# Kernel tuning notes

Measured on AMD Instinct MI355X. Metric: run time of the kernel, lower is better.

Reference implementation:

```python
import jax, jax.numpy as jnp
import numpy as np

K = 3
STRIDE = 2
SQRT_D = 4  # in_d_capsules = 16 -> 4x4 matrix pose
LN_EPS = 1e-5


def _unfold(x, k, s):
    # x: [B, N, H, W, A] -> [B, N, k, k, Hout, Wout, A] (matches torch unfold+permute)
    B, N, H, W, A = x.shape
    Hout = (H - k) // s + 1
    Wout = (W - k) // s + 1
    hi = jnp.arange(Hout) * s
    wi = jnp.arange(Wout) * s
    x1 = x[:, :, hi[:, None] + jnp.arange(k)[None, :]]            # [B,N,Hout,k,W,A]
    x2 = x1[:, :, :, :, wi[:, None] + jnp.arange(k)[None, :]]     # [B,N,Hout,k,Wout,k,A]
    return jnp.transpose(x2, (0, 1, 3, 5, 2, 4, 6))               # [B,N,k,k,Hout,Wout,A]


def setup_inputs() -> dict:
    key = jax.random.key(0)
    k1, k2, k3 = jax.random.split(key, 3)
    B, N_in, H, W, D_in = 32, 32, 32, 32, 16
    N_out, D_out = 32, 16
    Hout = (H - K) // STRIDE + 1
    Wout = (W - K) // STRIDE + 1
    w_const = np.sqrt(N_out / (SQRT_D * N_in * K * K)).astype(np.float32)
    return {
        "input": jax.random.normal(k1, (B, N_in, H, W, D_in), dtype=jnp.float32),
        "next_capsule_value": jax.random.normal(k2, (B, N_out, Hout, Wout, D_out), dtype=jnp.float32),
        "w": w_const * jax.random.normal(k3, (K, K, N_in, SQRT_D, SQRT_D, N_out), dtype=jnp.float32),
        "gamma": jnp.ones((D_out,), dtype=jnp.float32),
        "beta": jnp.zeros((D_out,), dtype=jnp.float32),
        "num_iter": 1,
    }


def reference(input, next_capsule_value, w, gamma, beta, num_iter):
    out_d = SQRT_D * SQRT_D
    scale = 1.0 / np.sqrt(out_d).astype(np.float32)
    inp = _unfold(input, K, STRIDE)                                # [B,N,k,k,h,w,A]
    B, N, _, _, h, wd, A = inp.shape
    _inp = inp.reshape(B, N, K, K, h, wd, SQRT_D, SQRT_D)          # bnklhwax
    M = next_capsule_value.shape[1]
    ncv = next_capsule_value.reshape(B, M, h, wd, SQRT_D, SQRT_D)  # bmhwad
    # query-key routing logits
    qk = jnp.einsum('bnklhwax,klnxdm,bmhwad->bnklmhw', _inp, w, ncv) * scale
    qk = jax.nn.softmax(qk, axis=4)
    qk = qk / (jnp.sum(qk, axis=4, keepdims=True) + 1e-10)
    # value aggregation
    out = jnp.einsum('bnklmhw,bnklhwax,klnxdm->bmhwad', qk, _inp, w)
    out = out.reshape(B, M, h, wd, out_d)
    # dropout p=0 -> identity; LayerNorm over capsule dim
    mu = jnp.mean(out, axis=-1, keepdims=True)
    var = jnp.var(out, axis=-1, keepdims=True)
    out = (out - mu) / jnp.sqrt(var + LN_EPS) * gamma + beta
    return out
```

## Files before the change

### kernel.cpp

```cpp
#include <hip/hip_runtime.h>

#define HOUT 15
#define WOUT 15

typedef float v2 __attribute__((ext_vector_type(2)));

#define DPP_ADDF(x, ctrl) \
    ((x) + __builtin_bit_cast(float, __builtin_amdgcn_update_dpp( \
        0, __builtin_bit_cast(int, (x)), (ctrl), 0xF, 0xF, true)))

__global__ __launch_bounds__(256) void prep_w(const float* __restrict__ wt,
                                              float* __restrict__ w2)
{
    const int t  = blockIdx.x * 256 + threadIdx.x;
    const int d  = t & 3;
    const int m  = (t >> 2) & 31;
    const int x  = (t >> 7) & 3;
    const int r  = t >> 9;
    const int kl = r % 9;
    const int n  = r / 9;
    w2[t] = wt[((((kl * 32 + n) * 4 + x) * 4 + d) * 32) + m];
}

__global__ __launch_bounds__(128, 4) void caps_fused(
    const float* __restrict__ input,
    const float* __restrict__ ncv,
    const float* __restrict__ w2,
    const float* __restrict__ gamma,
    const float* __restrict__ beta,
    float* __restrict__ out)
{
    const int tid  = threadIdx.x;
    const int grp  = tid >> 5;
    const int lane = tid & 31;

    const int pos = blockIdx.x * 4 + grp;
    const int b   = pos / (HOUT * WOUT);
    const int hw  = pos % (HOUT * WOUT);
    const int h   = hw / WOUT;
    const int wo  = hw % WOUT;
    const int h0  = h * 2, w0 = wo * 2;

    const float* ncv_p = ncv + ((((size_t)b * 32 + lane) * HOUT + h) * WOUT + wo) * 16;
    v2 cv2[8];
#pragma unroll
    for (int j = 0; j < 8; ++j) cv2[j] = *(const v2*)(ncv_p + j * 2);

    v2 acc2[8];
#pragma unroll
    for (int j = 0; j < 8; ++j) acc2[j] = (v2){0.0f, 0.0f};

    const float* ip0 = input + ((((size_t)b * 32) * 32 + h0) * 32 + w0) * 16;
    const float* wp0 = w2 + lane * 4;

    for (int n = 0; n < 32; ++n) {
        const float* ipn = ip0 + (size_t)n * 16384;
        const float* wpn = wp0 + (size_t)n * 4608;

#pragma unroll
        for (int kl = 0; kl < 9; ++kl) {
            const int k = kl / 3, l = kl % 3;
            const float* ip = ipn + (k * 32 + l) * 16;

            float av[16];
#pragma unroll
            for (int j = 0; j < 16; j += 4) {
                float4 t4 = *(const float4*)(ip + j);
                av[j] = t4.x; av[j + 1] = t4.y; av[j + 2] = t4.z; av[j + 3] = t4.w;
            }

            const float* wp = wpn + kl * 512;
            float4 wx[4];
#pragma unroll
            for (int x = 0; x < 4; ++x) wx[x] = *(const float4*)(wp + x * 128);

            v2 u2[8];
#pragma unroll
            for (int x = 0; x < 4; ++x) {
                v2 wlo = {wx[x].x, wx[x].y};
                v2 whi = {wx[x].z, wx[x].w};
#pragma unroll
                for (int a = 0; a < 4; ++a) {
                    v2 sp = {av[a * 4 + x], av[a * 4 + x]};
                    if (x == 0) {
                        u2[a * 2]     = sp * wlo;
                        u2[a * 2 + 1] = sp * whi;
                    } else {
                        u2[a * 2]     = __builtin_elementwise_fma(sp, wlo, u2[a * 2]);
                        u2[a * 2 + 1] = __builtin_elementwise_fma(sp, whi, u2[a * 2 + 1]);
                    }
                }
            }

            v2 d0 = {0.f, 0.f}, d1 = {0.f, 0.f};
#pragma unroll
            for (int j = 0; j < 4; ++j) {
                d0 = __builtin_elementwise_fma(u2[j],     cv2[j],     d0);
                d1 = __builtin_elementwise_fma(u2[j + 4], cv2[j + 4], d1);
            }
            v2 dd = d0 + d1;
            float e = __builtin_exp2f((dd.x + dd.y) * 0.36067376022224085f);

            float s = e;
            s = DPP_ADDF(s, 0xB1);
            s = DPP_ADDF(s, 0x4E);
            s = DPP_ADDF(s, 0x141);
            s = DPP_ADDF(s, 0x140);
            s += __builtin_bit_cast(float,
                  __builtin_amdgcn_ds_swizzle(__builtin_bit_cast(int, s), 0x401F));

            float p = e * __builtin_amdgcn_rcpf(s);
            v2 p2 = {p, p};
#pragma unroll
            for (int j = 0; j < 8; ++j)
                acc2[j] = __builtin_elementwise_fma(p2, u2[j], acc2[j]);
        }
    }

    v2 sv = acc2[0];
#pragma unroll
    for (int j = 1; j < 8; ++j) sv = sv + acc2[j];
    float mu = (sv.x + sv.y) * 0.0625f;
    v2 mv = {mu, mu};
    v2 vv = {0.f, 0.f};
#pragma unroll
    for (int j = 0; j < 8; ++j) {
        v2 dlt = acc2[j] - mv;
        vv = __builtin_elementwise_fma(dlt, dlt, vv);
    }
    float var  = (vv.x + vv.y) * 0.0625f;
    float rstd = __builtin_amdgcn_rsqf(var + 1e-5f);

    float* op = out + ((((size_t)b * 32 + lane) * HOUT + h) * WOUT + wo) * 16;
#pragma unroll
    for (int j = 0; j < 4; ++j) {
        float4 g  = *(const float4*)(gamma + j * 4);
        float4 be = *(const float4*)(beta  + j * 4);
        float4 r;
        r.x = (acc2[2 * j].x     - mu) * rstd * g.x + be.x;
        r.y = (acc2[2 * j].y     - mu) * rstd * g.y + be.y;
        r.z = (acc2[2 * j + 1].x - mu) * rstd * g.z + be.z;
        r.w = (acc2[2 * j + 1].y - mu) * rstd * g.w + be.w;
        *(float4*)(op + j * 4) = r;
    }
}

extern "C" void kernel_launch(void* const* d_in, const int* in_sizes, int n_in,
                              void* d_out, int out_size, void* d_ws, size_t ws_size,
                              hipStream_t stream) {
    const float* input = (const float*)d_in[0];
    const float* ncv   = (const float*)d_in[1];
    const float* wt    = (const float*)d_in[2];
    const float* gamma = (const float*)d_in[3];
    const float* beta  = (const float*)d_in[4];
    float* out = (float*)d_out;
    float* w2  = (float*)d_ws;

    prep_w<<<dim3(576), dim3(256), 0, stream>>>(wt, w2);
    caps_fused<<<dim3(1800), dim3(128), 0, stream>>>(input, ncv, w2, gamma, beta, out);
}
```

Before: 386.6 us.

## Split input-capsule reduction across two blocks and add separate LayerNorm pass

The fused kernel is split so each block handles half of the 32 input capsules (blockIdx.y), doubling the grid to 3600 blocks. Each half writes its partial sum, one into the output buffer and one into workspace. A new kernel then adds the two partials and applies LayerNorm. Launch bounds also rise to 7 waves per SIMD to raise occupancy. This adds an extra launch and partial-sum memory traffic in return for more parallelism and better latency hiding.

After: 1.162 ms. 200% more time.

```diff
diff --git a/kernel.cpp b/kernel.cpp
--- a/kernel.cpp
+++ b/kernel.cpp
@@ -22,13 +22,12 @@
     w2[t] = wt[((((kl * 32 + n) * 4 + x) * 4 + d) * 32) + m];
 }
 
-__global__ __launch_bounds__(128, 4) void caps_fused(
+__global__ __launch_bounds__(128, 7) void caps_part(
     const float* __restrict__ input,
     const float* __restrict__ ncv,
     const float* __restrict__ w2,
-    const float* __restrict__ gamma,
-    const float* __restrict__ beta,
-    float* __restrict__ out)
+    float* __restrict__ part0,
+    float* __restrict__ part1)
 {
     const int tid  = threadIdx.x;
     const int grp  = tid >> 5;
@@ -41,6 +40,8 @@
     const int wo  = hw % WOUT;
     const int h0  = h * 2, w0 = wo * 2;
 
+    const int n0 = blockIdx.y * 16;
+
     const float* ncv_p = ncv + ((((size_t)b * 32 + lane) * HOUT + h) * WOUT + wo) * 16;
     v2 cv2[8];
 #pragma unroll
@@ -50,12 +51,12 @@
 #pragma unroll
     for (int j = 0; j < 8; ++j) acc2[j] = (v2){0.0f, 0.0f};
 
-    const float* ip0 = input + ((((size_t)b * 32) * 32 + h0) * 32 + w0) * 16;
-    const float* wp0 = w2 + lane * 4;
+    const float* ip0 = input + ((((size_t)b * 32 + n0) * 32 + h0) * 32 + w0) * 16;
+    const float* wp0 = w2 + (size_t)n0 * 4608 + lane * 4;
 
-    for (int n = 0; n < 32; ++n) {
-        const float* ipn = ip0 + (size_t)n * 16384;
-        const float* wpn = wp0 + (size_t)n * 4608;
+    for (int ni = 0; ni < 16; ++ni) {
+        const float* ipn = ip0 + (size_t)ni * 16384;
+        const float* wpn = wp0 + (size_t)ni * 4608;
 
 #pragma unroll
         for (int kl = 0; kl < 9; ++kl) {
@@ -117,31 +118,56 @@
         }
     }
 
-    v2 sv = acc2[0];
+    float* op = (blockIdx.y == 0 ? part0 : part1)
+              + ((((size_t)b * 32 + lane) * HOUT + h) * WOUT + wo) * 16;
 #pragma unroll
-    for (int j = 1; j < 8; ++j) sv = sv + acc2[j];
-    float mu = (sv.x + sv.y) * 0.0625f;
-    v2 mv = {mu, mu};
-    v2 vv = {0.f, 0.f};
+    for (int j = 0; j < 4; ++j) {
+        float4 r;
+        r.x = acc2[2 * j].x;     r.y = acc2[2 * j].y;
+        r.z = acc2[2 * j + 1].x; r.w = acc2[2 * j + 1].y;
+        *(float4*)(op + j * 4) = r;
+    }
+}
+
+__global__ __launch_bounds__(256) void caps_ln(
+    const float* __restrict__ part1,
+    const float* __restrict__ gamma,
+    const float* __restrict__ beta,
+    float* __restrict__ out)
+{
+    const size_t t = (size_t)blockIdx.x * 256 + threadIdx.x;
+    const float* p0 = out   + t * 16;
+    const float* p1 = part1 + t * 16;
+
+    float a[16];
 #pragma unroll
-    for (int j = 0; j < 8; ++j) {
-        v2 dlt = acc2[j] - mv;
-        vv = __builtin_elementwise_fma(dlt, dlt, vv);
+    for (int j = 0; j < 16; j += 4) {
+        float4 x = *(const float4*)(p0 + j);
+        float4 y = *(const float4*)(p1 + j);
+        a[j] = x.x + y.x; a[j+1] = x.y + y.y; a[j+2] = x.z + y.z; a[j+3] = x.w + y.w;
     }
-    float var  = (vv.x + vv.y) * 0.0625f;
+
+    float mu = 0.0f;
+#pragma unroll
+    for (int j = 0; j < 16; ++j) mu += a[j];
+    mu *= 0.0625f;
+    float var = 0.0f;
+#pragma unroll
+    for (int j = 0; j < 16; ++j) { float d = a[j] - mu; var = fmaf(d, d, var); }
+    var *= 0.0625f;
     float rstd = __builtin_amdgcn_rsqf(var + 1e-5f);
 
-    float* op = out + ((((size_t)b * 32 + lane) * HOUT + h) * WOUT + wo) * 16;
+    float* op = out + t * 16;
 #pragma unroll
-    for (int j = 0; j < 4; ++j) {
-        float4 g  = *(const float4*)(gamma + j * 4);
-        float4 be = *(const float4*)(beta  + j * 4);
+    for (int j = 0; j < 16; j += 4) {
+        float4 g  = *(const float4*)(gamma + j);
+        float4 be = *(const float4*)(beta + j);
         float4 r;
-        r.x = (acc2[2 * j].x     - mu) * rstd * g.x + be.x;
-        r.y = (acc2[2 * j].y     - mu) * rstd * g.y + be.y;
-        r.z = (acc2[2 * j + 1].x - mu) * rstd * g.z + be.z;
-        r.w = (acc2[2 * j + 1].y - mu) * rstd * g.w + be.w;
-        *(float4*)(op + j * 4) = r;
+        r.x = (a[j + 0] - mu) * rstd * g.x + be.x;
+        r.y = (a[j + 1] - mu) * rstd * g.y + be.y;
+        r.z = (a[j + 2] - mu) * rstd * g.z + be.z;
+        r.w = (a[j + 3] - mu) * rstd * g.w + be.w;
+        *(float4*)(op + j) = r;
     }
 }
 
@@ -155,7 +181,9 @@
     const float* beta  = (const float*)d_in[4];
     float* out = (float*)d_out;
     float* w2  = (float*)d_ws;
+    float* p1  = (float*)d_ws + 147456;
 
     prep_w<<<dim3(576), dim3(256), 0, stream>>>(wt, w2);
-    caps_fused<<<dim3(1800), dim3(128), 0, stream>>>(input, ncv, w2, gamma, beta, out);
+    caps_part<<<dim3(1800, 2), dim3(128), 0, stream>>>(input, ncv, w2, out, p1);
+    caps_ln<<<dim3(900), dim3(256), 0, stream>>>(p1, gamma, beta, out);
 }
```

## Split each output capsule across two lanes using full 64-wide wavefronts

Applied to the files above, without the earlier changes.

Each output position now gets a full 64-lane wavefront instead of 32 lanes. Each output capsule m is split across two half-waves that each compute half of the d dimension, and the partial logits and LayerNorm statistics are combined with a cross-half shuffle. The weights are re-laid-out so each lane loads two float4s per kernel tap, and the softmax scale is folded into the ncv values. The intent is to halve per-thread registers and FMA work so more threads run in parallel. The cost is extra shuffles and input loads that are duplicated across the two halves.

Measured after the change: 356.7 us. 1.08x faster.

```diff
diff --git a/kernel.cpp b/kernel.cpp
--- a/kernel.cpp
+++ b/kernel.cpp
@@ -10,98 +10,101 @@
         0, __builtin_bit_cast(int, (x)), (ctrl), 0xF, 0xF, true)))
 
 __global__ __launch_bounds__(256) void prep_w(const float* __restrict__ wt,
-                                              float* __restrict__ w2)
+                                              float* __restrict__ w3)
 {
-    const int t  = blockIdx.x * 256 + threadIdx.x;
-    const int d  = t & 3;
-    const int m  = (t >> 2) & 31;
-    const int x  = (t >> 7) & 3;
-    const int r  = t >> 9;
-    const int kl = r % 9;
-    const int n  = r / 9;
-    w2[t] = wt[((((kl * 32 + n) * 4 + x) * 4 + d) * 32) + m];
+    const int t   = blockIdx.x * 256 + threadIdx.x;
+    const int e   = t & 3;
+    const int l64 = (t >> 2) & 63;
+    const int xq  = (t >> 8) & 1;
+    const int r   = t >> 9;
+    const int kl  = r % 9;
+    const int n   = r / 9;
+    const int mm  = l64 & 31;
+    const int hf  = l64 >> 5;
+    const int x   = 2 * xq + (e >> 1);
+    const int d   = 2 * hf + (e & 1);
+    w3[t] = wt[((kl * 32 + n) * 16 + x * 4 + d) * 32 + mm];
 }
 
-__global__ __launch_bounds__(128, 4) void caps_fused(
+__global__ __launch_bounds__(256) void caps_all(
     const float* __restrict__ input,
     const float* __restrict__ ncv,
-    const float* __restrict__ w2,
+    const float* __restrict__ w3,
     const float* __restrict__ gamma,
     const float* __restrict__ beta,
     float* __restrict__ out)
 {
     const int tid  = threadIdx.x;
-    const int grp  = tid >> 5;
-    const int lane = tid & 31;
+    const int l64  = tid & 63;
+    const int m    = l64 & 31;
+    const int half = l64 >> 5;
 
-    const int pos = blockIdx.x * 4 + grp;
-    const int b   = pos / (HOUT * WOUT);
-    const int hw  = pos % (HOUT * WOUT);
-    const int h   = hw / WOUT;
-    const int wo  = hw % WOUT;
-    const int h0  = h * 2, w0 = wo * 2;
+    const int posu = __builtin_amdgcn_readfirstlane(blockIdx.x * 4 + (tid >> 6));
+    const int b  = posu / (HOUT * WOUT);
+    const int hw = posu % (HOUT * WOUT);
+    const int h  = hw / WOUT;
+    const int wo = hw % WOUT;
 
-    const float* ncv_p = ncv + ((((size_t)b * 32 + lane) * HOUT + h) * WOUT + wo) * 16;
-    v2 cv2[8];
-#pragma unroll
-    for (int j = 0; j < 8; ++j) cv2[j] = *(const v2*)(ncv_p + j * 2);
+    const float* ipb = input + (size_t)b * 524288 + (h * 2) * 512 + (wo * 2) * 16;
 
-    v2 acc2[8];
-#pragma unroll
-    for (int j = 0; j < 8; ++j) acc2[j] = (v2){0.0f, 0.0f};
+    const float* cvp = ncv + (((size_t)b * 32 + m) * (HOUT * WOUT) + hw) * 16 + 2 * half;
+    const float SC = 0.36067376022224085f;
+    v2 sc2 = {SC, SC};
+    v2 cv0 = *(const v2*)(cvp +  0) * sc2;
+    v2 cv1 = *(const v2*)(cvp +  4) * sc2;
+    v2 cv2 = *(const v2*)(cvp +  8) * sc2;
+    v2 cv3 = *(const v2*)(cvp + 12) * sc2;
 
-    const float* ip0 = input + ((((size_t)b * 32) * 32 + h0) * 32 + w0) * 16;
-    const float* wp0 = w2 + lane * 4;
+    v2 acc0 = {0.f, 0.f}, acc1 = {0.f, 0.f}, acc2 = {0.f, 0.f}, acc3 = {0.f, 0.f};
+
+    const float* wlane = w3 + l64 * 4;
 
     for (int n = 0; n < 32; ++n) {
-        const float* ipn = ip0 + (size_t)n * 16384;
-        const float* wpn = wp0 + (size_t)n * 4608;
+        const float* ipn = ipb + (size_t)n * 16384;
+        const float* wn  = wlane + (size_t)n * 4608;
 
 #pragma unroll
         for (int kl = 0; kl < 9; ++kl) {
             const int k = kl / 3, l = kl % 3;
-            const float* ip = ipn + (k * 32 + l) * 16;
 
-            float av[16];
-#pragma unroll
-            for (int j = 0; j < 16; j += 4) {
-                float4 t4 = *(const float4*)(ip + j);
-                av[j] = t4.x; av[j + 1] = t4.y; av[j + 2] = t4.z; av[j + 3] = t4.w;
-            }
+            const float* ap = ipn + k * 512 + l * 16;
+            const float4 a0 = *(const float4*)(ap + 0);
+            const float4 a1 = *(const float4*)(ap + 4);
+            const float4 a2 = *(const float4*)(ap + 8);
+            const float4 a3 = *(const float4*)(ap + 12);
 
-            const float* wp = wpn + kl * 512;
-            float4 wx[4];
-#pragma unroll
-            for (int x = 0; x < 4; ++x) wx[x] = *(const float4*)(wp + x * 128);
+            const float* wp = wn + kl * 512;
+            const float4 q0 = *(const float4*)(wp);
+            const float4 q1 = *(const float4*)(wp + 256);
+            const v2 wx0 = {q0.x, q0.y}, wx1 = {q0.z, q0.w};
+            const v2 wx2 = {q1.x, q1.y}, wx3 = {q1.z, q1.w};
 
-            v2 u2[8];
-#pragma unroll
-            for (int x = 0; x < 4; ++x) {
-                v2 wlo = {wx[x].x, wx[x].y};
-                v2 whi = {wx[x].z, wx[x].w};
-#pragma unroll
-                for (int a = 0; a < 4; ++a) {
-                    v2 sp = {av[a * 4 + x], av[a * 4 + x]};
-                    if (x == 0) {
-                        u2[a * 2]     = sp * wlo;
-                        u2[a * 2 + 1] = sp * whi;
-                    } else {
-                        u2[a * 2]     = __builtin_elementwise_fma(sp, wlo, u2[a * 2]);
-                        u2[a * 2 + 1] = __builtin_elementwise_fma(sp, whi, u2[a * 2 + 1]);
-                    }
-                }
-            }
+            v2 u0 = (v2){a0.x, a0.x} * wx0;
+            u0 = __builtin_elementwise_fma((v2){a0.y, a0.y}, wx1, u0);
+            u0 = __builtin_elementwise_fma((v2){a0.z, a0.z}, wx2, u0);
+            u0 = __builtin_elementwise_fma((v2){a0.w, a0.w}, wx3, u0);
+            v2 u1 = (v2){a1.x, a1.x} * wx0;
+            u1 = __builtin_elementwise_fma((v2){a1.y, a1.y}, wx1, u1);
+            u1 = __builtin_elementwise_fma((v2){a1.z, a1.z}, wx2, u1);
+            u1 = __builtin_elementwise_fma((v2){a1.w, a1.w}, wx3, u1);
+            v2 u2 = (v2){a2.x, a2.x} * wx0;
+            u2 = __builtin_elementwise_fma((v2){a2.y, a2.y}, wx1, u2);
+            u2 = __builtin_elementwise_fma((v2){a2.z, a2.z}, wx2, u2);
+            u2 = __builtin_elementwise_fma((v2){a2.w, a2.w}, wx3, u2);
+            v2 u3 = (v2){a3.x, a3.x} * wx0;
+            u3 = __builtin_elementwise_fma((v2){a3.y, a3.y}, wx1, u3);
+            u3 = __builtin_elementwise_fma((v2){a3.z, a3.z}, wx2, u3);
+            u3 = __builtin_elementwise_fma((v2){a3.w, a3.w}, wx3, u3);
 
-            v2 d0 = {0.f, 0.f}, d1 = {0.f, 0.f};
-#pragma unroll
-            for (int j = 0; j < 4; ++j) {
-                d0 = __builtin_elementwise_fma(u2[j],     cv2[j],     d0);
-                d1 = __builtin_elementwise_fma(u2[j + 4], cv2[j + 4], d1);
-            }
-            v2 dd = d0 + d1;
-            float e = __builtin_exp2f((dd.x + dd.y) * 0.36067376022224085f);
+            v2 ds = u0 * cv0;
+            ds = __builtin_elementwise_fma(u1, cv1, ds);
+            ds = __builtin_elementwise_fma(u2, cv2, ds);
+            ds = __builtin_elementwise_fma(u3, cv3, ds);
+            float part = ds.x + ds.y;
+            float lg   = part + __shfl_xor(part, 32, 64);
+            float e1   = __builtin_exp2f(lg);
 
-            float s = e;
+            float s = e1;
             s = DPP_ADDF(s, 0xB1);
             s = DPP_ADDF(s, 0x4E);
             s = DPP_ADDF(s, 0x141);
@@ -109,39 +112,52 @@
             s += __builtin_bit_cast(float,
                   __builtin_amdgcn_ds_swizzle(__builtin_bit_cast(int, s), 0x401F));
 
-            float p = e * __builtin_amdgcn_rcpf(s);
+            float p = e1 * __builtin_amdgcn_rcpf(s);
             v2 p2 = {p, p};
-#pragma unroll
-            for (int j = 0; j < 8; ++j)
-                acc2[j] = __builtin_elementwise_fma(p2, u2[j], acc2[j]);
+            acc0 = __builtin_elementwise_fma(p2, u0, acc0);
+            acc1 = __builtin_elementwise_fma(p2, u1, acc1);
+            acc2 = __builtin_elementwise_fma(p2, u2, acc2);
+            acc3 = __builtin_elementwise_fma(p2, u3, acc3);
         }
     }
 
-    v2 sv = acc2[0];
-#pragma unroll
-    for (int j = 1; j < 8; ++j) sv = sv + acc2[j];
-    float mu = (sv.x + sv.y) * 0.0625f;
+    v2 s2 = (acc0 + acc1) + (acc2 + acc3);
+    float s8  = s2.x + s2.y;
+    float s16 = s8 + __shfl_xor(s8, 32, 64);
+    float mu  = s16 * 0.0625f;
     v2 mv = {mu, mu};
+
     v2 vv = {0.f, 0.f};
-#pragma unroll
-    for (int j = 0; j < 8; ++j) {
-        v2 dlt = acc2[j] - mv;
-        vv = __builtin_elementwise_fma(dlt, dlt, vv);
+    v2 t0 = acc0 - mv; vv = __builtin_elementwise_fma(t0, t0, vv);
+    v2 t1 = acc1 - mv; vv = __builtin_elementwise_fma(t1, t1, vv);
+    v2 t2 = acc2 - mv; vv = __builtin_elementwise_fma(t2, t2, vv);
+    v2 t3 = acc3 - mv; vv = __builtin_elementwise_fma(t3, t3, vv);
+    float v8  = vv.x + vv.y;
+    float v16 = v8 + __shfl_xor(v8, 32, 64);
+    float rstd = __builtin_amdgcn_rsqf(v16 * 0.0625f + 1e-5f);
+    v2 rs2 = {rstd, rstd};
+
+    const int db = 2 * half;
+    float* op = out + (((size_t)b * 32 + m) * (HOUT * WOUT) + hw) * 16 + db;
+    {
+        v2 g  = *(const v2*)(gamma + 0 + db);
+        v2 be = *(const v2*)(beta  + 0 + db);
+        *(v2*)(op + 0)  = __builtin_elementwise_fma(t0 * rs2, g, be);
     }
-    float var  = (vv.x + vv.y) * 0.0625f;
-    float rstd = __builtin_amdgcn_rsqf(var + 1e-5f);
-
-    float* op = out + ((((size_t)b * 32 + lane) * HOUT + h) * WOUT + wo) * 16;
-#pragma unroll
-    for (int j = 0; j < 4; ++j) {
-        float4 g  = *(const float4*)(gamma + j * 4);
-        float4 be = *(const float4*)(beta  + j * 4);
-        float4 r;
-        r.x = (acc2[2 * j].x     - mu) * rstd * g.x + be.x;
-        r.y = (acc2[2 * j].y     - mu) * rstd * g.y + be.y;
-        r.z = (acc2[2 * j + 1].x - mu) * rstd * g.z + be.z;
-        r.w = (acc2[2 * j + 1].y - mu) * rstd * g.w + be.w;
-        *(float4*)(op + j * 4) = r;
+    {
+        v2 g  = *(const v2*)(gamma + 4 + db);
+        v2 be = *(const v2*)(beta  + 4 + db);
+        *(v2*)(op + 4)  = __builtin_elementwise_fma(t1 * rs2, g, be);
+    }
+    {
+        v2 g  = *(const v2*)(gamma + 8 + db);
+        v2 be = *(const v2*)(beta  + 8 + db);
+        *(v2*)(op + 8)  = __builtin_elementwise_fma(t2 * rs2, g, be);
+    }
+    {
+        v2 g  = *(const v2*)(gamma + 12 + db);
+        v2 be = *(const v2*)(beta  + 12 + db);
+        *(v2*)(op + 12) = __builtin_elementwise_fma(t3 * rs2, g, be);
     }
 }
 
@@ -154,8 +170,8 @@
     const float* gamma = (const float*)d_in[3];
     const float* beta  = (const float*)d_in[4];
     float* out = (float*)d_out;
-    float* w2  = (float*)d_ws;
+    float* w3  = (float*)d_ws;
 
-    prep_w<<<dim3(576), dim3(256), 0, stream>>>(wt, w2);
-    caps_fused<<<dim3(1800), dim3(128), 0, stream>>>(input, ncv, w2, gamma, beta, out);
+    prep_w<<<dim3(576), dim3(256), 0, stream>>>(wt, w3);
+    caps_all<<<dim3(1800), dim3(256), 0, stream>>>(input, ncv, w3, gamma, beta, out);
 }
```
